# Kernel optimization log

Hardware: AMD Instinct MI355X
Metric: run time of the kernel (lower is better)

The kernel has to match this reference:

```python
import jax, jax.numpy as jnp
import numpy as np

D_MODEL = 1024
N_HEADS = 16
D_K = D_MODEL // N_HEADS
SEQ = 2048
BATCH = 4


def setup_inputs() -> dict:
    key = jax.random.key(0)
    ks = jax.random.split(key, 11)
    s = 0.02
    inp = {
        'query': jax.random.normal(ks[0], (SEQ, BATCH, D_MODEL), jnp.float32),
        'key': jax.random.normal(ks[1], (SEQ, BATCH, D_MODEL), jnp.float32),
        'value': jax.random.normal(ks[2], (SEQ, BATCH, D_MODEL), jnp.float32),
        'Wq': jax.random.normal(ks[3], (D_MODEL, D_MODEL), jnp.float32) * s,
        'bq': jnp.zeros((D_MODEL,), jnp.float32),
        'Wk': jax.random.normal(ks[4], (D_MODEL, D_MODEL), jnp.float32) * s,
        'bk': jnp.zeros((D_MODEL,), jnp.float32),
        'Wv': jax.random.normal(ks[5], (D_MODEL, D_MODEL), jnp.float32) * s,
        'bv': jnp.zeros((D_MODEL,), jnp.float32),
        'Wo': jax.random.normal(ks[6], (D_MODEL, D_MODEL), jnp.float32) * s,
        'bo': jnp.zeros((D_MODEL,), jnp.float32),
    }
    return inp


def reference(query, key, value, Wq, bq, Wk, bk, Wv, bv, Wo, bo):
    # inputs are [S, B, D]; module transposes to batch-first
    q_in = jnp.swapaxes(query, 0, 1)  # [B, S, D]
    k_in = jnp.swapaxes(key, 0, 1)
    v_in = jnp.swapaxes(value, 0, 1)
    B, S, _ = q_in.shape
    # torch Linear: x @ W.T + b
    q = (q_in @ Wq.T + bq).reshape(B, S, N_HEADS, D_K)
    k = (k_in @ Wk.T + bk).reshape(B, S, N_HEADS, D_K)
    v = (v_in @ Wv.T + bv).reshape(B, S, N_HEADS, D_K)
    scale = jnp.sqrt(jnp.float32(D_K))
    scores = jnp.einsum('bqhd,bkhd->bhqk', q, k) / scale  # [B, H, S, S]
    attn = jax.nn.softmax(scores, axis=-1)
    # dropout is identity in eval / p=0
    context = jnp.einsum('bhqk,bkhd->bqhd', attn, v).reshape(B, S, D_MODEL)
    out = context @ Wo.T + bo  # [B, S, D]
    return jnp.swapaxes(out, 0, 1)  # back to [S, B, D]
```

## Files before the change

### kernel.cpp

```cpp
#include <hip/hip_runtime.h>
#include <math.h>

typedef unsigned short u16;
typedef unsigned int   u32;
typedef float f32x4 __attribute__((ext_vector_type(4)));
typedef __bf16 bf16x8 __attribute__((ext_vector_type(8)));

#define SEQ   2048
#define BATCH 4
#define NH    16
#define DK    64
#define DM    1024
#define MTOT  (SEQ*BATCH)
#define SCL_QK 0.18033688011116016f

static __device__ __forceinline__ u16 f2bf(float f) {
  __bf16 h = (__bf16)f;
  return __builtin_bit_cast(u16, h);
}
static __device__ __forceinline__ u32 pk2(float a, float b) {
  return (u32)f2bf(a) | ((u32)f2bf(b) << 16);
}

typedef __attribute__((address_space(1))) const void g1_t;
typedef __attribute__((address_space(3))) void l3_t;
static __device__ __forceinline__ void gload16(const void* g, void* l) {
  __builtin_amdgcn_global_load_lds((g1_t*)g, (l3_t*)l, 16, 0, 0);
}

__global__ __launch_bounds__(256)
void cast_bf16(const float* __restrict__ src, u16* __restrict__ dst, int n8) {
  int i = blockIdx.x * 256 + threadIdx.x;
  if (i < n8) {
    float4 a = ((const float4*)src)[2 * i];
    float4 b = ((const float4*)src)[2 * i + 1];
    uint4 r;
    r.x = pk2(a.x, a.y); r.y = pk2(a.z, a.w);
    r.z = pk2(b.x, b.y); r.w = pk2(b.z, b.w);
    ((uint4*)dst)[i] = r;
  }
}

template<int AMODE, int SMODE, int QSCALE>
__global__ __launch_bounds__(512, 4)
void gemm_bf16(const u16* __restrict__ A, const u16* __restrict__ W,
               const float* __restrict__ bias, void* __restrict__ outv)
{
  constexpr int BM = 128, BN = 128, BK = 32;
  __shared__ u16 As[BM * BK];
  __shared__ u16 Bs[BN * BK];

  const int m0 = blockIdx.y * BM;
  const int n0 = blockIdx.x * BN;
  const int tid  = threadIdx.x;
  const int w    = tid >> 6;
  const int lane = tid & 63;
  const int quad = lane >> 4;
  const int l15  = lane & 15;
  const int wm = (w & 1) * 64;
  const int wn = (w >> 1) * 32;

  const int srow = tid >> 2;
  const int scol = (tid & 3) * 8;
  size_t aoff;
  {
    int gm = m0 + srow;
    if (AMODE == 0) {
      int bb = gm >> 11, s = gm & (SEQ - 1);
      aoff = (size_t)(s * BATCH + bb) * DM + scol;
    } else {
      aoff = (size_t)gm * DM + scol;
    }
  }
  const size_t woff = (size_t)(n0 + srow) * DM + scol;
  u16* as_dst = &As[w * 16 * BK];
  u16* bs_dst = &Bs[w * 16 * BK];

  f32x4 zero4 = {0.f, 0.f, 0.f, 0.f};
  f32x4 acc[4][2];
  for (int i = 0; i < 4; i++)
    for (int j = 0; j < 2; j++)
      acc[i][j] = zero4;

  for (int k0 = 0; k0 < DM; k0 += BK) {
    gload16(A + aoff + k0, as_dst);
    gload16(W + woff + k0, bs_dst);
    __syncthreads();
    bf16x8 af[4], bfr[2];
    for (int i = 0; i < 4; i++)
      af[i] = *(const bf16x8*)&As[(wm + i * 16 + l15) * BK + quad * 8];
    for (int j = 0; j < 2; j++)
      bfr[j] = *(const bf16x8*)&Bs[(wn + j * 16 + l15) * BK + quad * 8];
    for (int i = 0; i < 4; i++)
      for (int j = 0; j < 2; j++)
        acc[i][j] = __builtin_amdgcn_mfma_f32_16x16x32_bf16(af[i], bfr[j], acc[i][j], 0, 0, 0);
    __syncthreads();
  }

  for (int j = 0; j < 2; j++) {
    int gn = n0 + wn + j * 16 + l15;
    float bv = bias[gn];
    for (int i = 0; i < 4; i++) {
      int gmb = m0 + wm + i * 16 + quad * 4;
      for (int r = 0; r < 4; r++) {
        int gm = gmb + r;
        float val = acc[i][j][r] + bv;
        if (QSCALE) val *= SCL_QK;
        int bb = gm >> 11, s = gm & (SEQ - 1);
        if (SMODE == 0) {
          int h = gn >> 6, dk = gn & 63;
          ((u16*)outv)[((size_t)(bb * NH + h) * SEQ + s) * DK + dk] = f2bf(val);
        } else if (SMODE == 1) {
          int h = gn >> 6, dk = gn & 63;
          ((u16*)outv)[((size_t)(bb * NH + h) * DK + dk) * SEQ + s] = f2bf(val);
        } else {
          ((float*)outv)[(size_t)(s * BATCH + bb) * DM + gn] = val;
        }
      }
    }
  }
}

__global__ __launch_bounds__(256, 4)
void attn3(const u16* __restrict__ Q, const u16* __restrict__ K,
           const u16* __restrict__ VT, u16* __restrict__ ctx)
{
  __shared__ u16 Ks[64 * 64];
  __shared__ u16 Vs[64 * 64];
  __shared__ u16 Ps[4][32][72];

  const int bh = blockIdx.x;
  const int qt = blockIdx.y;
  const int b  = bh >> 4, h = bh & 15;
  const int tid  = threadIdx.x;
  const int w    = tid >> 6;
  const int lane = tid & 63;
  const int quad = lane >> 4;
  const int l15  = lane & 15;

  const u16* Qb = Q  + (size_t)bh * SEQ * DK;
  const u16* Kb = K  + (size_t)bh * SEQ * DK;
  const u16* Vb = VT + (size_t)bh * DK * SEQ;

  const int qbase = qt * 128 + w * 32;
  bf16x8 qf[2][2];
  for (int qh = 0; qh < 2; qh++)
    for (int kc = 0; kc < 2; kc++)
      qf[qh][kc] = *(const bf16x8*)&Qb[(size_t)(qbase + qh * 16 + l15) * DK + kc * 32 + quad * 8];

  float lsum[2] = {0.f, 0.f};
  f32x4 zero4 = {0.f, 0.f, 0.f, 0.f};
  f32x4 ot[2][4];
  for (int qh = 0; qh < 2; qh++)
    for (int fn = 0; fn < 4; fn++) ot[qh][fn] = zero4;

  const int r0 = tid >> 3;
  const int sw = (tid & 7) ^ (r0 & 7);
  const int s3 = l15 & 7;
  const int c0 = ((0 + quad) ^ s3) * 8;
  const int c1 = ((4 + quad) ^ s3) * 8;

  for (int kb = 0; kb < SEQ / 64; kb++) {
    __syncthreads();
    for (int p = 0; p < 2; p++) {
      int row = p * 32 + r0;
      gload16(&Kb[(size_t)(kb * 64 + row) * DK + sw * 8], &Ks[(p * 32 + w * 8) * 64]);
      gload16(&Vb[(size_t)row * SEQ + kb * 64 + sw * 8], &Vs[(p * 32 + w * 8) * 64]);
    }
    __syncthreads();

    f32x4 st[2][4];
    for (int qh = 0; qh < 2; qh++)
      for (int fn = 0; fn < 4; fn++) st[qh][fn] = zero4;
    for (int kc = 0; kc < 2; kc++)
      for (int fn = 0; fn < 4; fn++) {
        bf16x8 kf = *(const bf16x8*)&Ks[(fn * 16 + l15) * 64 + (kc ? c1 : c0)];
        for (int qh = 0; qh < 2; qh++)
          st[qh][fn] = __builtin_amdgcn_mfma_f32_16x16x32_bf16(kf, qf[qh][kc], st[qh][fn], 0, 0, 0);
      }

    for (int qh = 0; qh < 2; qh++) {
      float part = 0.f;
      for (int fn = 0; fn < 4; fn++)
        for (int r = 0; r < 4; r++) {
          float p = exp2f(fminf(st[qh][fn][r], 120.f));
          st[qh][fn][r] = p;
          part += p;
        }
      lsum[qh] += part;
    }

    for (int qh = 0; qh < 2; qh++)
      for (int fn = 0; fn < 4; fn++) {
        uint2 pr;
        pr.x = pk2(st[qh][fn][0], st[qh][fn][1]);
        pr.y = pk2(st[qh][fn][2], st[qh][fn][3]);
        *(uint2*)&Ps[w][qh * 16 + l15][fn * 16 + quad * 4] = pr;
      }

    for (int kc = 0; kc < 2; kc++) {
      bf16x8 pf[2];
      for (int qh = 0; qh < 2; qh++)
        pf[qh] = *(const bf16x8*)&Ps[w][qh * 16 + l15][kc * 32 + quad * 8];
      for (int fn = 0; fn < 4; fn++) {
        bf16x8 vf = *(const bf16x8*)&Vs[(fn * 16 + l15) * 64 + (kc ? c1 : c0)];
        for (int qh = 0; qh < 2; qh++)
          ot[qh][fn] = __builtin_amdgcn_mfma_f32_16x16x32_bf16(vf, pf[qh], ot[qh][fn], 0, 0, 0);
      }
    }
  }

  for (int qh = 0; qh < 2; qh++) {
    float l = lsum[qh];
    l += __shfl_xor(l, 16);
    l += __shfl_xor(l, 32);
    float inv = 1.0f / l;
    int qg = qbase + qh * 16 + l15;
    for (int fn = 0; fn < 4; fn++) {
      uint2 pr;
      pr.x = pk2(ot[qh][fn][0] * inv, ot[qh][fn][1] * inv);
      pr.y = pk2(ot[qh][fn][2] * inv, ot[qh][fn][3] * inv);
      *(uint2*)&ctx[((size_t)(b * SEQ + qg)) * DM + h * DK + fn * 16 + quad * 4] = pr;
    }
  }
}

extern "C" void kernel_launch(void* const* d_in, const int* in_sizes, int n_in,
                              void* d_out, int out_size, void* d_ws, size_t ws_size,
                              hipStream_t stream)
{
  const float* q  = (const float*)d_in[0];
  const float* k  = (const float*)d_in[1];
  const float* v  = (const float*)d_in[2];
  const float* Wq = (const float*)d_in[3];
  const float* bq = (const float*)d_in[4];
  const float* Wk = (const float*)d_in[5];
  const float* bk = (const float*)d_in[6];
  const float* Wv = (const float*)d_in[7];
  const float* bv = (const float*)d_in[8];
  const float* Wo = (const float*)d_in[9];
  const float* bo = (const float*)d_in[10];

  u16* in_c  = (u16*)d_ws;
  u16* w_c   = in_c  + (size_t)MTOT * DM;
  u16* q_ws  = w_c   + (size_t)DM * DM;
  u16* k_ws  = q_ws  + (size_t)MTOT * DM;
  u16* vt_ws = k_ws  + (size_t)MTOT * DM;
  u16* ctx   = in_c;

  const int NA8 = MTOT * DM / 8;
  const int NW8 = DM * DM / 8;
  dim3 cblk(256);
  dim3 gblk(512);
  dim3 gg(DM / 128, MTOT / 128);

  cast_bf16<<<NA8 / 256, cblk, 0, stream>>>(q, in_c, NA8);
  cast_bf16<<<NW8 / 256, cblk, 0, stream>>>(Wq, w_c, NW8);
  gemm_bf16<0, 0, 1><<<gg, gblk, 0, stream>>>(in_c, w_c, bq, q_ws);

  cast_bf16<<<NA8 / 256, cblk, 0, stream>>>(k, in_c, NA8);
  cast_bf16<<<NW8 / 256, cblk, 0, stream>>>(Wk, w_c, NW8);
  gemm_bf16<0, 0, 0><<<gg, gblk, 0, stream>>>(in_c, w_c, bk, k_ws);

  cast_bf16<<<NA8 / 256, cblk, 0, stream>>>(v, in_c, NA8);
  cast_bf16<<<NW8 / 256, cblk, 0, stream>>>(Wv, w_c, NW8);
  gemm_bf16<0, 1, 0><<<gg, gblk, 0, stream>>>(in_c, w_c, bv, vt_ws);

  attn3<<<dim3(BATCH * NH, SEQ / 128), cblk, 0, stream>>>(q_ws, k_ws, vt_ws, ctx);

  cast_bf16<<<NW8 / 256, cblk, 0, stream>>>(Wo, w_c, NW8);
  gemm_bf16<1, 3, 0><<<gg, gblk, 0, stream>>>(ctx, w_c, bo, d_out);
}
```

Baseline: 419.1 us.

## Batch casts and QKV projections into single launches, retile GEMM to 256 threads

Merges all fp32→bf16 casts into one launch and the three Q/K/V projections into one grid over a segment index, which removes many small launches and fills the GPU better. The GEMM now uses 256 threads with each wave computing a 64x64 tile (4x4 MFMA accumulators), and it loads two rows per thread. The bf16 pair packing uses a vector conversion, and the exp2 clamp in attention is dropped. This needs a larger workspace, with a fallback path for smaller ones. Removing the clamp risks overflow on inputs with large scores.

```diff
diff --git a/kernel.cpp b/kernel.cpp
--- a/kernel.cpp
+++ b/kernel.cpp
@@ -5,6 +5,7 @@
 typedef unsigned int   u32;
 typedef float f32x4 __attribute__((ext_vector_type(4)));
 typedef __bf16 bf16x8 __attribute__((ext_vector_type(8)));
+typedef __bf16 bf16x2 __attribute__((ext_vector_type(2)));
 
 #define SEQ   2048
 #define BATCH 4
@@ -19,7 +20,8 @@
   return __builtin_bit_cast(u16, h);
 }
 static __device__ __forceinline__ u32 pk2(float a, float b) {
-  return (u32)f2bf(a) | ((u32)f2bf(b) << 16);
+  bf16x2 t = {(__bf16)a, (__bf16)b};
+  return __builtin_bit_cast(u32, t);
 }
 
 typedef __attribute__((address_space(1))) const void g1_t;
@@ -28,93 +30,136 @@
   __builtin_amdgcn_global_load_lds((g1_t*)g, (l3_t*)l, 16, 0, 0);
 }
 
+static __device__ __forceinline__ void cast8(const float* __restrict__ src,
+                                             u16* __restrict__ dst, int i) {
+  float4 a = ((const float4*)src)[2 * i];
+  float4 b = ((const float4*)src)[2 * i + 1];
+  uint4 r;
+  r.x = pk2(a.x, a.y); r.y = pk2(a.z, a.w);
+  r.z = pk2(b.x, b.y); r.w = pk2(b.z, b.w);
+  ((uint4*)dst)[i] = r;
+}
+
 __global__ __launch_bounds__(256)
 void cast_bf16(const float* __restrict__ src, u16* __restrict__ dst, int n8) {
   int i = blockIdx.x * 256 + threadIdx.x;
-  if (i < n8) {
-    float4 a = ((const float4*)src)[2 * i];
-    float4 b = ((const float4*)src)[2 * i + 1];
-    uint4 r;
-    r.x = pk2(a.x, a.y); r.y = pk2(a.z, a.w);
-    r.z = pk2(b.x, b.y); r.w = pk2(b.z, b.w);
-    ((uint4*)dst)[i] = r;
-  }
-}
-
-template<int AMODE, int SMODE, int QSCALE>
-__global__ __launch_bounds__(512, 4)
-void gemm_bf16(const u16* __restrict__ A, const u16* __restrict__ W,
-               const float* __restrict__ bias, void* __restrict__ outv)
+  if (i < n8) cast8(src, dst, i);
+}
+
+__global__ __launch_bounds__(256)
+void cast_w(const float* __restrict__ Wq, const float* __restrict__ Wk,
+            const float* __restrict__ Wv, const float* __restrict__ Wo,
+            u16* __restrict__ w3, u16* __restrict__ wo_c) {
+  int bid = blockIdx.x;
+  int t = bid >> 9, idx = bid & 511;
+  const float* src = (t == 0) ? Wq : (t == 1) ? Wk : (t == 2) ? Wv : Wo;
+  u16* dst = (t < 3) ? (w3 + (size_t)t * DM * DM) : wo_c;
+  cast8(src, dst, idx * 256 + threadIdx.x);
+}
+
+__global__ __launch_bounds__(256)
+void cast_all(const float* __restrict__ q, const float* __restrict__ k,
+              const float* __restrict__ v,
+              const float* __restrict__ Wq, const float* __restrict__ Wk,
+              const float* __restrict__ Wv, const float* __restrict__ Wo,
+              u16* __restrict__ in_c, u16* __restrict__ w3, u16* __restrict__ wo_c) {
+  int bid = blockIdx.x;
+  const float* src; u16* dst; int idx;
+  if (bid < 12288) {
+    int t = bid >> 12; idx = bid & 4095;
+    src = (t == 0) ? q : (t == 1) ? k : v;
+    dst = in_c + (size_t)t * MTOT * DM;
+  } else {
+    int wb = bid - 12288;
+    int t = wb >> 9; idx = wb & 511;
+    src = (t == 0) ? Wq : (t == 1) ? Wk : (t == 2) ? Wv : Wo;
+    dst = (t < 3) ? (w3 + (size_t)t * DM * DM) : wo_c;
+  }
+  cast8(src, dst, idx * 256 + threadIdx.x);
+}
+
+template<int OGEMM>
+__global__ __launch_bounds__(256, 4)
+void gemm_k(const u16* __restrict__ a0, const u16* __restrict__ a1,
+            const u16* __restrict__ a2, const u16* __restrict__ w3,
+            const float* __restrict__ b0, const float* __restrict__ b1,
+            const float* __restrict__ b2,
+            u16* __restrict__ o0, u16* __restrict__ o1, u16* __restrict__ o2,
+            float* __restrict__ o3, int seg_base)
 {
   constexpr int BM = 128, BN = 128, BK = 32;
   __shared__ u16 As[BM * BK];
   __shared__ u16 Bs[BN * BK];
 
-  const int m0 = blockIdx.y * BM;
-  const int n0 = blockIdx.x * BN;
+  const int seg = OGEMM ? 0 : (seg_base + (int)(blockIdx.x >> 3));
+  const int n0  = OGEMM ? blockIdx.x * BN : (blockIdx.x & 7) * BN;
+  const int m0  = blockIdx.y * BM;
+  const u16* A = OGEMM ? a0 : (seg == 0 ? a0 : seg == 1 ? a1 : a2);
+  const u16* W = OGEMM ? w3 : (w3 + (size_t)seg * DM * DM);
+  const float* bias = OGEMM ? b0 : (seg == 0 ? b0 : seg == 1 ? b1 : b2);
+
   const int tid  = threadIdx.x;
   const int w    = tid >> 6;
   const int lane = tid & 63;
   const int quad = lane >> 4;
   const int l15  = lane & 15;
-  const int wm = (w & 1) * 64;
-  const int wn = (w >> 1) * 32;
-
-  const int srow = tid >> 2;
-  const int scol = (tid & 3) * 8;
-  size_t aoff;
-  {
-    int gm = m0 + srow;
-    if (AMODE == 0) {
+  const int wm = (w >> 1) * 64;
+  const int wn = (w & 1) * 64;
+
+  size_t aoff[2], woff[2];
+  for (int p = 0; p < 2; p++) {
+    int row = w * 32 + p * 16 + (lane >> 2);
+    int gm = m0 + row;
+    if (OGEMM) {
+      aoff[p] = (size_t)gm * DM + (lane & 3) * 8;
+    } else {
       int bb = gm >> 11, s = gm & (SEQ - 1);
-      aoff = (size_t)(s * BATCH + bb) * DM + scol;
-    } else {
-      aoff = (size_t)gm * DM + scol;
-    }
-  }
-  const size_t woff = (size_t)(n0 + srow) * DM + scol;
-  u16* as_dst = &As[w * 16 * BK];
-  u16* bs_dst = &Bs[w * 16 * BK];
+      aoff[p] = (size_t)(s * BATCH + bb) * DM + (lane & 3) * 8;
+    }
+    woff[p] = (size_t)(n0 + row) * DM + (lane & 3) * 8;
+  }
 
   f32x4 zero4 = {0.f, 0.f, 0.f, 0.f};
-  f32x4 acc[4][2];
+  f32x4 acc[4][4];
   for (int i = 0; i < 4; i++)
-    for (int j = 0; j < 2; j++)
+    for (int j = 0; j < 4; j++)
       acc[i][j] = zero4;
 
   for (int k0 = 0; k0 < DM; k0 += BK) {
-    gload16(A + aoff + k0, as_dst);
-    gload16(W + woff + k0, bs_dst);
+    for (int p = 0; p < 2; p++) {
+      gload16(A + aoff[p] + k0, &As[(w * 32 + p * 16) * BK]);
+      gload16(W + woff[p] + k0, &Bs[(w * 32 + p * 16) * BK]);
+    }
     __syncthreads();
-    bf16x8 af[4], bfr[2];
+    bf16x8 af[4], bfr[4];
     for (int i = 0; i < 4; i++)
       af[i] = *(const bf16x8*)&As[(wm + i * 16 + l15) * BK + quad * 8];
-    for (int j = 0; j < 2; j++)
+    for (int j = 0; j < 4; j++)
       bfr[j] = *(const bf16x8*)&Bs[(wn + j * 16 + l15) * BK + quad * 8];
     for (int i = 0; i < 4; i++)
-      for (int j = 0; j < 2; j++)
+      for (int j = 0; j < 4; j++)
         acc[i][j] = __builtin_amdgcn_mfma_f32_16x16x32_bf16(af[i], bfr[j], acc[i][j], 0, 0, 0);
     __syncthreads();
   }
 
-  for (int j = 0; j < 2; j++) {
+  for (int j = 0; j < 4; j++) {
     int gn = n0 + wn + j * 16 + l15;
     float bv = bias[gn];
+    int h = gn >> 6, dk = gn & 63;
     for (int i = 0; i < 4; i++) {
       int gmb = m0 + wm + i * 16 + quad * 4;
       for (int r = 0; r < 4; r++) {
         int gm = gmb + r;
         float val = acc[i][j][r] + bv;
-        if (QSCALE) val *= SCL_QK;
         int bb = gm >> 11, s = gm & (SEQ - 1);
-        if (SMODE == 0) {
-          int h = gn >> 6, dk = gn & 63;
-          ((u16*)outv)[((size_t)(bb * NH + h) * SEQ + s) * DK + dk] = f2bf(val);
-        } else if (SMODE == 1) {
-          int h = gn >> 6, dk = gn & 63;
-          ((u16*)outv)[((size_t)(bb * NH + h) * DK + dk) * SEQ + s] = f2bf(val);
+        if (OGEMM) {
+          o3[(size_t)(s * BATCH + bb) * DM + gn] = val;
+        } else if (seg == 0) {
+          o0[((size_t)(bb * NH + h) * SEQ + s) * DK + dk] = f2bf(val * SCL_QK);
+        } else if (seg == 1) {
+          o1[((size_t)(bb * NH + h) * SEQ + s) * DK + dk] = f2bf(val);
         } else {
-          ((float*)outv)[(size_t)(s * BATCH + bb) * DM + gn] = val;
+          o2[((size_t)(bb * NH + h) * DK + dk) * SEQ + s] = f2bf(val);
         }
       }
     }
@@ -183,7 +228,7 @@
       float part = 0.f;
       for (int fn = 0; fn < 4; fn++)
         for (int r = 0; r < 4; r++) {
-          float p = exp2f(fminf(st[qh][fn][r], 120.f));
+          float p = exp2f(st[qh][fn][r]);
           st[qh][fn][r] = p;
           part += p;
         }
@@ -241,33 +286,53 @@
   const float* Wo = (const float*)d_in[9];
   const float* bo = (const float*)d_in[10];
 
-  u16* in_c  = (u16*)d_ws;
-  u16* w_c   = in_c  + (size_t)MTOT * DM;
-  u16* q_ws  = w_c   + (size_t)DM * DM;
-  u16* k_ws  = q_ws  + (size_t)MTOT * DM;
-  u16* vt_ws = k_ws  + (size_t)MTOT * DM;
-  u16* ctx   = in_c;
-
-  const int NA8 = MTOT * DM / 8;
-  const int NW8 = DM * DM / 8;
+  const size_t SZ_IN  = (size_t)MTOT * DM;
+  const size_t SZ_W   = (size_t)DM * DM;
+  const size_t NEED_FUSED = (3 * SZ_IN + 3 * SZ_W + SZ_W + 3 * SZ_IN) * 2;
+
   dim3 cblk(256);
-  dim3 gblk(512);
-  dim3 gg(DM / 128, MTOT / 128);
-
-  cast_bf16<<<NA8 / 256, cblk, 0, stream>>>(q, in_c, NA8);
-  cast_bf16<<<NW8 / 256, cblk, 0, stream>>>(Wq, w_c, NW8);
-  gemm_bf16<0, 0, 1><<<gg, gblk, 0, stream>>>(in_c, w_c, bq, q_ws);
-
-  cast_bf16<<<NA8 / 256, cblk, 0, stream>>>(k, in_c, NA8);
-  cast_bf16<<<NW8 / 256, cblk, 0, stream>>>(Wk, w_c, NW8);
-  gemm_bf16<0, 0, 0><<<gg, gblk, 0, stream>>>(in_c, w_c, bk, k_ws);
-
-  cast_bf16<<<NA8 / 256, cblk, 0, stream>>>(v, in_c, NA8);
-  cast_bf16<<<NW8 / 256, cblk, 0, stream>>>(Wv, w_c, NW8);
-  gemm_bf16<0, 1, 0><<<gg, gblk, 0, stream>>>(in_c, w_c, bv, vt_ws);
-
-  attn3<<<dim3(BATCH * NH, SEQ / 128), cblk, 0, stream>>>(q_ws, k_ws, vt_ws, ctx);
-
-  cast_bf16<<<NW8 / 256, cblk, 0, stream>>>(Wo, w_c, NW8);
-  gemm_bf16<1, 3, 0><<<gg, gblk, 0, stream>>>(ctx, w_c, bo, d_out);
-}
+  dim3 ggq(24, 64);
+  dim3 ggs(8, 64);
+
+  if (ws_size >= NEED_FUSED) {
+    u16* in_c  = (u16*)d_ws;
+    u16* w3    = in_c + 3 * SZ_IN;
+    u16* wo_c  = w3   + 3 * SZ_W;
+    u16* q_ws  = wo_c + SZ_W;
+    u16* k_ws  = q_ws + SZ_IN;
+    u16* vt_ws = k_ws + SZ_IN;
+    u16* ctx   = in_c;
+
+    cast_all<<<14336, cblk, 0, stream>>>(q, k, v, Wq, Wk, Wv, Wo, in_c, w3, wo_c);
+    gemm_k<0><<<ggq, cblk, 0, stream>>>(in_c, in_c + SZ_IN, in_c + 2 * SZ_IN, w3,
+                                        bq, bk, bv, q_ws, k_ws, vt_ws, nullptr, 0);
+    attn3<<<dim3(BATCH * NH, SEQ / 128), cblk, 0, stream>>>(q_ws, k_ws, vt_ws, ctx);
+    gemm_k<1><<<ggs, cblk, 0, stream>>>(ctx, ctx, ctx, wo_c,
+                                        bo, bo, bo, nullptr, nullptr, nullptr,
+                                        (float*)d_out, 0);
+  } else {
+    u16* in_c  = (u16*)d_ws;
+    u16* w3    = in_c + SZ_IN;
+    u16* wo_c  = w3   + 3 * SZ_W;
+    u16* q_ws  = wo_c + SZ_W;
+    u16* k_ws  = q_ws + SZ_IN;
+    u16* vt_ws = k_ws + SZ_IN;
+    u16* ctx   = in_c;
+
+    const int NA8 = MTOT * DM / 8;
+    cast_w<<<2048, cblk, 0, stream>>>(Wq, Wk, Wv, Wo, w3, wo_c);
+    cast_bf16<<<NA8 / 256, cblk, 0, stream>>>(q, in_c, NA8);
+    gemm_k<0><<<ggs, cblk, 0, stream>>>(in_c, in_c, in_c, w3, bq, bk, bv,
+                                        q_ws, k_ws, vt_ws, nullptr, 0);
+    cast_bf16<<<NA8 / 256, cblk, 0, stream>>>(k, in_c, NA8);
+    gemm_k<0><<<ggs, cblk, 0, stream>>>(in_c, in_c, in_c, w3, bq, bk, bv,
+                                        q_ws, k_ws, vt_ws, nullptr, 1);
+    cast_bf16<<<NA8 / 256, cblk, 0, stream>>>(v, in_c, NA8);
+    gemm_k<0><<<ggs, cblk, 0, stream>>>(in_c, in_c, in_c, w3, bq, bk, bv,
+                                        q_ws, k_ws, vt_ws, nullptr, 2);
+    attn3<<<dim3(BATCH * NH, SEQ / 128), cblk, 0, stream>>>(q_ws, k_ws, vt_ws, ctx);
+    gemm_k<1><<<ggs, cblk, 0, stream>>>(ctx, ctx, ctx, wo_c,
+                                        bo, bo, bo, nullptr, nullptr, nullptr,
+                                        (float*)d_out, 0);
+  }
+}
```

New measurement: 402.7 us. 1.04x faster.
